# Kernel optimization log

Measured on AMD Instinct MI355X. Metric: run time of the kernel, lower is better.

## Reference

```python
import jax, jax.numpy as jnp
import numpy as np

DIM = 1024
HEADS = 16
DHEAD = 64
MAXLEN = 512
B = 8
N = 256   # sequence (x) length
M = 256   # memory (h) length; M + N <= MAXLEN
INNER = HEADS * DHEAD


def setup_inputs() -> dict:
    key = jax.random.key(0)
    ks = jax.random.split(key, 8)
    w = lambda k, shape: jax.random.normal(k, shape, jnp.float32) * 0.02
    return {
        "x": jax.random.normal(ks[0], (B, N, DIM), jnp.float32),
        "h": jax.random.normal(ks[1], (B, M, DIM), jnp.float32),
        "Wqkv": w(ks[2], (DIM, 3 * INNER)),
        "Wkr": w(ks[3], (DIM, INNER)),
        "R": jax.random.normal(ks[4], (2 * MAXLEN, DIM), jnp.float32),
        "u": jax.random.normal(ks[5], (DHEAD,), jnp.float32),
        "v": jax.random.normal(ks[6], (DHEAD,), jnp.float32),
        "Wout": w(ks[7], (INNER, DIM)),
        "max_len": MAXLEN,
    }


def reference(x, h, Wqkv, Wkr, R, u, v, Wout, max_len):
    b, n, dim = x.shape
    m = h.shape[1]
    t = m + n
    scale = DHEAD ** -0.5

    cat = jnp.concatenate([h, x], axis=1)                     # [b, t, dim]
    qkv = cat @ Wqkv                                          # [b, t, 3*inner]
    q, k, val = [s.reshape(b, t, HEADS, DHEAD).transpose(0, 2, 1, 3)
                 for s in jnp.split(qkv, 3, axis=-1)]          # [b, h, t, d]

    # shifts[i, j] = (j - i) mod 2L, sliced as in the torch buffer
    ar = jnp.arange(2 * max_len)
    shifts_full = (ar[None, :] - ar[:, None]) % (2 * max_len)
    shifts = shifts_full[:max_len, :max_len][m:m + n, :t]      # [n, t]

    kr = (R @ Wkr)[shifts]                                    # gather: [n, t, inner]
    kr = kr.reshape(n, t, HEADS, DHEAD).transpose(2, 0, 1, 3)  # [h, n, t, d]

    q = q[:, :, m:]                                           # [b, h, n, d]

    term_a = jnp.einsum('bhnd,bhmd->bhnm', q, k)
    term_b = jnp.einsum('bhnd,hnmd->bhnm', q, kr)
    term_c = jnp.einsum('d,bhmd->bhm', u, k)[:, :, None, :]    # broadcast over n
    term_d = jnp.einsum('d,hnmd->hnm', v, kr)[None]            # broadcast over b
    dots = (term_a + term_b + term_c + term_d) * scale         # [b, h, n, t]

    qi = jnp.arange(n)[:, None]
    jm = jnp.arange(m)[None, :]
    js = jnp.arange(n)[None, :]
    mem_mask = jnp.where(qi > jm, -jnp.inf, 0.0)               # [n, m]
    ar_mask = jnp.where(js > qi, -jnp.inf, 0.0)                # [n, n]
    bias = jnp.concatenate([mem_mask, ar_mask], axis=1)[None, None]  # [1,1,n,t]

    attn = jax.nn.softmax(dots + bias, axis=-1)
    out = jnp.einsum('bhnm,bhmd->bhnd', attn, val)             # [b, h, n, d]
    out = out.transpose(0, 2, 1, 3).reshape(b, n, INNER)
    return out @ Wout
```

## Files before the change

kernel.cpp:

```cpp
#include <hip/hip_runtime.h>
#include <hip/hip_bf16.h>
#include <math.h>

typedef unsigned short u16;
typedef short bf16x8 __attribute__((ext_vector_type(8)));
typedef float f32x4 __attribute__((ext_vector_type(4)));

__device__ __forceinline__ u16 f2b(float f) {
    __hip_bfloat16 h = __float2bfloat16(f);
    return *reinterpret_cast<u16*>(&h);
}
__device__ __forceinline__ float b2f(u16 v) {
    __hip_bfloat16 h;
    *reinterpret_cast<u16*>(&h) = v;
    return __bfloat162float(h);
}

__device__ __forceinline__ void gload_lds16(const void* g, void* l) {
    __builtin_amdgcn_global_load_lds(
        (const __attribute__((address_space(1))) void*)g,
        (__attribute__((address_space(3))) void*)l, 16, 0, 0);
}


struct EpiQKV4 {
    u16 *Q, *Kt, *Vt;
    __device__ void operator()(int rowp, int colp, f32x4 vals) const {
        int b = colp >> 9, pos = colp & 511;
        int sec = rowp >> 10, cc = rowp & 1023;
        int head = cc >> 6, d0 = cc & 63;
        ushort4 o;
        if (sec == 0) {
            if (pos < 256) return;
            o.x = f2b(vals[0] * 0.125f); o.y = f2b(vals[1] * 0.125f);
            o.z = f2b(vals[2] * 0.125f); o.w = f2b(vals[3] * 0.125f);
            *(ushort4*)(Q + (long)((head * 8 + b) * 256 + (pos - 256)) * 64 + d0) = o;
        } else {
            u16* dst = (sec == 1) ? Kt : Vt;
            o.x = f2b(vals[0]); o.y = f2b(vals[1]);
            o.z = f2b(vals[2]); o.w = f2b(vals[3]);
            *(ushort4*)(dst + (long)((b * 16 + head) * 512 + pos) * 64 + d0) = o;
        }
    }
};

struct EpiStoreBf {
    u16* C; long ldc; long strideZ;
    __device__ void operator()(int z, int row, int col, float val) const {
        C[(long)z * strideZ + (long)row * ldc + col] = f2b(val);
    }
};

struct EpiStoreF32 {
    float* C; long ldc;
    __device__ void operator()(int z, int row, int col, float val) const {
        C[(long)row * ldc + col] = val;
    }
};


template <typename Epi, bool AF32, bool ADDA, bool ROWMAP>
__device__ __forceinline__ void gemm_bt_body(char* smem, int bx, int by, int bz,
                                             const void* __restrict__ Av, int lda, long strideAz,
                                             const u16* __restrict__ B, int ldb, long strideBz,
                                             int K, Epi epi, const float* __restrict__ av) {
    constexpr int LDT = 56;
    u16* As = (u16*)smem;
    u16* Bs = As + 64 * LDT;
    int n0 = bx * 64, m0 = by * 64, z = bz;
    const u16* Bb = B + (long)z * strideBz + (long)n0 * ldb;
    int tid = threadIdx.x;
    int wave = tid >> 6, lane = tid & 63;
    int wm = wave >> 1, wn = wave & 1;
    int lrow = lane & 15, lquad = lane >> 4;
    int srow = tid >> 2, scol = (tid & 3) * 8;
    f32x4 acc[2][2] = {};
    for (int k0 = 0; k0 < K; k0 += 32) {
        if constexpr (AF32) {
            long arow = m0 + srow;
            if constexpr (ROWMAP) arow = (arow < 256) ? 768 + arow : 0;
            const float* src = (const float*)Av + (long)z * strideAz + arow * lda + k0 + scol;
            float4 f0 = *(const float4*)src;
            float4 f1 = *(const float4*)(src + 4);
            bf16x8 vv;
            vv[0] = (short)f2b(f0.x); vv[1] = (short)f2b(f0.y);
            vv[2] = (short)f2b(f0.z); vv[3] = (short)f2b(f0.w);
            vv[4] = (short)f2b(f1.x); vv[5] = (short)f2b(f1.y);
            vv[6] = (short)f2b(f1.z); vv[7] = (short)f2b(f1.w);
            *(bf16x8*)(As + srow * LDT + scol) = vv;
        } else {
            const u16* Ab = (const u16*)Av + (long)z * strideAz + (long)m0 * lda;
            *(bf16x8*)(As + srow * LDT + scol) = *(const bf16x8*)(Ab + (long)srow * lda + k0 + scol);
        }
        *(bf16x8*)(Bs + srow * LDT + scol) = *(const bf16x8*)(Bb + (long)srow * ldb + k0 + scol);
        __syncthreads();
        bf16x8 af[2], bfr[2];
        #pragma unroll
        for (int mt = 0; mt < 2; ++mt) {
            af[mt] = *(const bf16x8*)(As + (wm * 32 + mt * 16 + lrow) * LDT + lquad * 8);
            if constexpr (ADDA) {
                #pragma unroll
                for (int j = 0; j < 8; ++j)
                    af[mt][j] = (short)f2b(b2f((u16)af[mt][j]) + 0.125f * av[k0 + lquad * 8 + j]);
            }
        }
        #pragma unroll
        for (int nt = 0; nt < 2; ++nt)
            bfr[nt] = *(const bf16x8*)(Bs + (wn * 32 + nt * 16 + lrow) * LDT + lquad * 8);
        #pragma unroll
        for (int mt = 0; mt < 2; ++mt)
            #pragma unroll
            for (int nt = 0; nt < 2; ++nt)
                acc[mt][nt] = __builtin_amdgcn_mfma_f32_16x16x32_bf16(af[mt], bfr[nt], acc[mt][nt], 0, 0, 0);
        __syncthreads();
    }
    #pragma unroll
    for (int mt = 0; mt < 2; ++mt)
        #pragma unroll
        for (int nt = 0; nt < 2; ++nt)
            #pragma unroll
            for (int r = 0; r < 4; ++r) {
                int row = m0 + wm * 32 + mt * 16 + lquad * 4 + r;
                int col = n0 + wn * 32 + nt * 16 + lrow;
                epi(z, row, col, acc[mt][nt][r]);
            }
}

__global__ __launch_bounds__(256) void prep_kernel(const float* __restrict__ x,
                                                   const float* __restrict__ h,
                                                   u16* __restrict__ catBF,
                                                   const float* __restrict__ Wqkv, u16* __restrict__ WqkvT,
                                                   const float* __restrict__ Wkr,  u16* __restrict__ WkrT,
                                                   const float* __restrict__ Wout, u16* __restrict__ WoutT) {
    __shared__ float tile[32][33];
    int bid = blockIdx.x, tid = threadIdx.x;
    if (bid < 2048) {
        int idx = (bid * 256 + tid) * 8;
        int c = idx & 1023, r = idx >> 10;
        int b = r >> 9, pos = r & 511;
        const float* src = (pos < 256) ? h + ((long)(b * 256 + pos) * 1024 + c)
                                       : x + ((long)(b * 256 + pos - 256) * 1024 + c);
        float4 f0 = *(const float4*)src;
        float4 f1 = *(const float4*)(src + 4);
        bf16x8 vv;
        vv[0] = (short)f2b(f0.x); vv[1] = (short)f2b(f0.y);
        vv[2] = (short)f2b(f0.z); vv[3] = (short)f2b(f0.w);
        vv[4] = (short)f2b(f1.x); vv[5] = (short)f2b(f1.y);
        vv[6] = (short)f2b(f1.z); vv[7] = (short)f2b(f1.w);
        *(bf16x8*)(catBF + idx) = vv;
        return;
    }
    const float* W; u16* WT; int nb, kb;
    if (bid < 5120) {
        int w = bid - 2048;
        W = Wqkv; WT = WqkvT;
        nb = (w % 96) * 32; kb = (w / 96) * 32;
        int tx = tid & 31, ty = tid >> 5;
        #pragma unroll
        for (int i = 0; i < 32; i += 8)
            tile[ty + i][tx] = W[(long)(kb + ty + i) * 3072 + nb + tx];
    } else {
        int w = bid - 5120;
        if (w < 1024) { W = Wkr; WT = WkrT; }
        else          { W = Wout; WT = WoutT; w -= 1024; }
        nb = (w & 31) * 32; kb = (w >> 5) * 32;
        int tx = tid & 31, ty = tid >> 5;
        #pragma unroll
        for (int i = 0; i < 32; i += 8)
            tile[ty + i][tx] = W[(long)(kb + ty + i) * 1024 + nb + tx];
    }
    __syncthreads();
    int row = tid >> 3;
    int c4 = (tid & 7) * 4;
    ushort4 o;
    o.x = f2b(tile[c4 + 0][row]);
    o.y = f2b(tile[c4 + 1][row]);
    o.z = f2b(tile[c4 + 2][row]);
    o.w = f2b(tile[c4 + 3][row]);
    *(ushort4*)(WT + (long)(nb + row) * 1024 + kb + c4) = o;
}

__global__ __launch_bounds__(256) void qkv_rwg_kernel(const u16* __restrict__ A, const u16* __restrict__ B,
                                                      EpiQKV4 eq,
                                                      const float* __restrict__ R, const u16* __restrict__ WkrT,
                                                      u16* __restrict__ RWg) {
    __shared__ alignas(16) char smem[32768];
    int bid = blockIdx.x;
    if (bid >= 768) {
        int bid2 = bid - 768;
        gemm_bt_body<EpiStoreBf, true, false, true>(smem, bid2 & 15, bid2 >> 4, 0,
            (const void*)R, 1024, 0L, WkrT, 1024, 0L, 1024, EpiStoreBf{RWg, 1024, 0}, nullptr);
        return;
    }
    int n0 = (bid & 31) * 128, m0 = (bid >> 5) * 128;
    u16* As = (u16*)smem;
    u16* Bs = As + 8192;
    int tid = threadIdx.x, wave = tid >> 6, lane = tid & 63;
    int wm = wave >> 1, wn = wave & 1;
    int lrow = lane & 15, lquad = lane >> 4;
    const u16* Ab = A + (long)m0 * 1024;
    const u16* Bb = B + (long)n0 * 1024;
    f32x4 acc[4][4] = {};
    for (int k0 = 0; k0 < 1024; k0 += 64) {
        #pragma unroll
        for (int i = 0; i < 4; ++i) {
            int rowb = (i & 1) * 64 + (tid >> 2);
            int col = k0 + (i >> 1) * 32 + (tid & 3) * 8;
            gload_lds16(Ab + (long)rowb * 1024 + col, As + i * 2048 + tid * 8);
            gload_lds16(Bb + (long)rowb * 1024 + col, Bs + i * 2048 + tid * 8);
        }
        __syncthreads();
        #pragma unroll
        for (int ks = 0; ks < 2; ++ks) {
            bf16x8 af[4], bfr[4];
            #pragma unroll
            for (int mt = 0; mt < 4; ++mt)
                af[mt] = *(const bf16x8*)(As + ks * 4096 + (wm * 64 + mt * 16 + lrow) * 32 + lquad * 8);
            #pragma unroll
            for (int nt = 0; nt < 4; ++nt)
                bfr[nt] = *(const bf16x8*)(Bs + ks * 4096 + (wn * 64 + nt * 16 + lrow) * 32 + lquad * 8);
            #pragma unroll
            for (int mt = 0; mt < 4; ++mt)
                #pragma unroll
                for (int nt = 0; nt < 4; ++nt)
                    acc[mt][nt] = __builtin_amdgcn_mfma_f32_16x16x32_bf16(af[mt], bfr[nt], acc[mt][nt], 0, 0, 0);
        }
        __syncthreads();
    }
    #pragma unroll
    for (int mt = 0; mt < 4; ++mt)
        #pragma unroll
        for (int nt = 0; nt < 4; ++nt) {
            int rowp = m0 + wm * 64 + mt * 16 + lquad * 4;
            int colp = n0 + wn * 64 + nt * 16 + lrow;
            eq(rowp, colp, acc[mt][nt]);
        }
}

__global__ __launch_bounds__(256) void vtrans_qr_kernel(const u16* __restrict__ Vtmp, u16* __restrict__ VT,
                                                        const u16* __restrict__ Q, const u16* __restrict__ RWg,
                                                        u16* __restrict__ QR, const float* __restrict__ v) {
    __shared__ alignas(16) char smem[14336];
    int bid = blockIdx.x, tid = threadIdx.x;
    if (bid < 4096) {
        u16 (*tile)[34] = (u16(*)[34])smem;
        int t0 = (bid & 15) * 32, d0 = ((bid >> 4) & 1) * 32, bh = bid >> 5;
        int tx = tid & 31, ty = tid >> 5;
        const u16* src = Vtmp + (long)bh * 512 * 64;
        #pragma unroll
        for (int i = 0; i < 32; i += 8)
            tile[ty + i][tx] = src[(long)(t0 + ty + i) * 64 + d0 + tx];
        __syncthreads();
        u16* dst = VT + (long)bh * 64 * 512;
        #pragma unroll
        for (int i = 0; i < 32; i += 8)
            dst[(long)(d0 + ty + i) * 512 + t0 + tx] = tile[tx][ty + i];
        return;
    }
    int bid2 = bid - 4096;
    int bx = bid2 % 5;
    int rest = bid2 / 5;
    int by = rest & 31, bz = rest >> 5;
    gemm_bt_body<EpiStoreBf, false, true, false>(smem, bx, by, bz,
        (const void*)Q, 64, 2048L * 64, RWg, 1024, 64L, 64,
        EpiStoreBf{QR, 320, 2048L * 320}, v);
}

__global__ __launch_bounds__(256) void outproj_kernel(const u16* __restrict__ A,
                                                      const u16* __restrict__ B,
                                                      float* __restrict__ out) {
    __shared__ alignas(16) char smem[14336];
    gemm_bt_body<EpiStoreF32, false, false, false>(smem, blockIdx.x, blockIdx.y, 0,
        (const void*)A, 1024, 0L, B, 1024, 0L, 1024, EpiStoreF32{out, 1024}, nullptr);
}

__global__ __launch_bounds__(256, 4) void attn_kernel(const u16* __restrict__ Qs,
                                                      const u16* __restrict__ Kt,
                                                      const u16* __restrict__ VT,
                                                      const u16* __restrict__ QR,
                                                      const float* __restrict__ uvec,
                                                      u16* __restrict__ attnOut) {
    constexpr int LDSW = 328;
    __shared__ alignas(16) u16 SQ[32 * LDSW];
    __shared__ float red[2][4][32];
    int id = blockIdx.x;
    int bh = id & 127, it = id >> 7;
    int b = bh >> 4, h = bh & 15;
    int i0 = it * 32;
    int w0 = i0;
    int tid = threadIdx.x, wave = tid >> 6, lane = tid & 63;
    int lrow = lane & 15, lquad = lane >> 4;

    const u16* qrg = QR + ((long)h * 2048 + b * 256 + i0) * 320;
    #pragma unroll
    for (int kk = 0; kk < 5; ++kk) {
        int idx = tid + kk * 256;
        int row = idx / 40, c = idx - row * 40;
        *(bf16x8*)(SQ + row * LDSW + c * 8) = *(const bf16x8*)(qrg + row * 320 + c * 8);
    }

    bf16x8 aq[2][2];
    #pragma unroll
    for (int iu = 0; iu < 2; ++iu) {
        const u16* qbase = Qs + (long)((h * 8 + b) * 256 + i0 + iu * 16 + lrow) * 64;
        aq[iu][0] = *(const bf16x8*)(qbase + lquad * 8);
        aq[iu][1] = *(const bf16x8*)(qbase + 32 + lquad * 8);
        #pragma unroll
        for (int j = 0; j < 8; ++j) {
            aq[iu][0][j] = (short)f2b(b2f((u16)aq[iu][0][j]) + 0.125f * uvec[lquad * 8 + j]);
            aq[iu][1][j] = (short)f2b(b2f((u16)aq[iu][1][j]) + 0.125f * uvec[32 + lquad * 8 + j]);
        }
    }

    const u16* kbase = Kt + ((long)bh * 512 + w0 + wave * 80) * 64;
    bf16x8 bk0[5], bk1[5];
    #pragma unroll
    for (int t = 0; t < 5; ++t) {
        const u16* kp = kbase + (long)(t * 16 + lrow) * 64;
        bk0[t] = *(const bf16x8*)(kp + lquad * 8);
        bk1[t] = *(const bf16x8*)(kp + 32 + lquad * 8);
    }
    f32x4 acc[2][5];
    #pragma unroll
    for (int t = 0; t < 5; ++t)
        #pragma unroll
        for (int iu = 0; iu < 2; ++iu) {
            f32x4 a = {0.f, 0.f, 0.f, 0.f};
            a = __builtin_amdgcn_mfma_f32_16x16x32_bf16(aq[iu][0], bk0[t], a, 0, 0, 0);
            a = __builtin_amdgcn_mfma_f32_16x16x32_bf16(aq[iu][1], bk1[t], a, 0, 0, 0);
            acc[iu][t] = a;
        }
    __syncthreads();

    float m4[2][4];
    #pragma unroll
    for (int iu = 0; iu < 2; ++iu)
        #pragma unroll
        for (int r = 0; r < 4; ++r) m4[iu][r] = -1e30f;
    #pragma unroll
    for (int t = 0; t < 5; ++t) {
        int lj = wave * 80 + t * 16 + lrow;
        #pragma unroll
        for (int iu = 0; iu < 2; ++iu)
            #pragma unroll
            for (int r = 0; r < 4; ++r) {
                int rloc = iu * 16 + lquad * 4 + r;
                int d = lj - rloc;
                int dc = d < 0 ? 0 : (d > 256 ? 256 : d);
                bool ok = (unsigned)d <= 256u;
                float val = ok ? acc[iu][t][r] + b2f(SQ[rloc * LDSW + dc]) : -1e30f;
                acc[iu][t][r] = val;
                m4[iu][r] = fmaxf(m4[iu][r], val);
            }
    }
    #pragma unroll
    for (int iu = 0; iu < 2; ++iu)
        #pragma unroll
        for (int r = 0; r < 4; ++r) {
            #pragma unroll
            for (int off = 1; off < 16; off <<= 1)
                m4[iu][r] = fmaxf(m4[iu][r], __shfl_xor(m4[iu][r], off));
            if (lrow == 0) red[0][wave][iu * 16 + lquad * 4 + r] = m4[iu][r];
        }
    __syncthreads();

    float gmax[2][4];
    #pragma unroll
    for (int iu = 0; iu < 2; ++iu)
        #pragma unroll
        for (int r = 0; r < 4; ++r) {
            int row = iu * 16 + lquad * 4 + r;
            gmax[iu][r] = fmaxf(fmaxf(red[0][0][row], red[0][1][row]),
                                fmaxf(red[0][2][row], red[0][3][row]));
        }

    float s4[2][4] = {};
    #pragma unroll
    for (int t = 0; t < 5; ++t) {
        int lj = wave * 80 + t * 16 + lrow;
        #pragma unroll
        for (int iu = 0; iu < 2; ++iu)
            #pragma unroll
            for (int r = 0; r < 4; ++r) {
                float p = __expf(acc[iu][t][r] - gmax[iu][r]);
                s4[iu][r] += p;
                SQ[(iu * 16 + lquad * 4 + r) * LDSW + lj] = f2b(p);
            }
    }
    #pragma unroll
    for (int iu = 0; iu < 2; ++iu)
        #pragma unroll
        for (int r = 0; r < 4; ++r) {
            #pragma unroll
            for (int off = 1; off < 16; off <<= 1)
                s4[iu][r] += __shfl_xor(s4[iu][r], off);
            if (lrow == 0) red[1][wave][iu * 16 + lquad * 4 + r] = s4[iu][r];
        }
    __syncthreads();

    const u16* vbase = VT + ((long)bh * 64 + wave * 16 + lrow) * 512 + w0;
    f32x4 oacc[2] = {};
    bf16x8 vp[10];
    #pragma unroll
    for (int t = 0; t < 10; ++t)
        vp[t] = *(const bf16x8*)(vbase + t * 32 + lquad * 8);
    #pragma unroll
    for (int t = 0; t < 10; ++t)
        #pragma unroll
        for (int iu = 0; iu < 2; ++iu) {
            bf16x8 ap = *(const bf16x8*)(SQ + (iu * 16 + lrow) * LDSW + t * 32 + lquad * 8);
            oacc[iu] = __builtin_amdgcn_mfma_f32_16x16x32_bf16(ap, vp[t], oacc[iu], 0, 0, 0);
        }
    #pragma unroll
    for (int iu = 0; iu < 2; ++iu)
        #pragma unroll
        for (int r = 0; r < 4; ++r) {
            int row = iu * 16 + lquad * 4 + r;
            float inv = 1.0f / (red[1][0][row] + red[1][1][row] + red[1][2][row] + red[1][3][row]);
            attnOut[(long)(b * 256 + i0 + row) * 1024 + h * 64 + wave * 16 + lrow] = f2b(oacc[iu][r] * inv);
        }
}


extern "C" void kernel_launch(void* const* d_in, const int* in_sizes, int n_in,
                              void* d_out, int out_size, void* d_ws, size_t ws_size,
                              hipStream_t stream) {
    (void)in_sizes; (void)n_in; (void)out_size; (void)ws_size;
    const float* x    = (const float*)d_in[0];
    const float* h    = (const float*)d_in[1];
    const float* Wqkv = (const float*)d_in[2];
    const float* Wkr  = (const float*)d_in[3];
    const float* R    = (const float*)d_in[4];
    const float* u    = (const float*)d_in[5];
    const float* v    = (const float*)d_in[6];
    const float* Wout = (const float*)d_in[7];
    float* out = (float*)d_out;

    char* ws = (char*)d_ws;
    size_t off = 0;
    auto alloc = [&](size_t bytes) -> void* {
        void* p = ws + off;
        off = (off + bytes + 255) & ~(size_t)255;
        return p;
    };
    u16* catBF  = (u16*)alloc(4096L * 1024 * 2);
    u16* WqkvT  = (u16*)alloc(3072L * 1024 * 2);
    u16* WkrT   = (u16*)alloc(1024L * 1024 * 2);
    u16* WoutT  = (u16*)alloc(1024L * 1024 * 2);
    u16* RWg    = (u16*)alloc(320L * 1024 * 2);
    u16* Q      = (u16*)alloc(16L * 8 * 256 * 64 * 2);
    u16* Kt     = (u16*)alloc(8L * 16 * 512 * 64 * 2);
    u16* Vtmp   = (u16*)alloc(8L * 16 * 512 * 64 * 2);
    u16* VT     = (u16*)alloc(8L * 16 * 64 * 512 * 2);
    u16* QR     = (u16*)alloc(16L * 2048 * 320 * 2);
    u16* attnO  = (u16*)alloc(2048L * 1024 * 2);

    prep_kernel<<<7168, 256, 0, stream>>>(x, h, catBF, Wqkv, WqkvT, Wkr, WkrT, Wout, WoutT);
    qkv_rwg_kernel<<<848, 256, 0, stream>>>(WqkvT, catBF, EpiQKV4{Q, Kt, Vtmp}, R, WkrT, RWg);
    vtrans_qr_kernel<<<6656, 256, 0, stream>>>(Vtmp, VT, Q, RWg, QR, v);
    attn_kernel<<<1024, 256, 0, stream>>>(Q, Kt, VT, QR, u, attnO);
    outproj_kernel<<<dim3(16, 32), 256, 0, stream>>>(attnO, WoutT, out);
}
```

Baseline: 194.3 us.

## Skip unused memory-token Q tiles, double-buffer QKV GEMM, swizzle blocks

The QKV GEMM now computes the Q projection only for the sequence tokens, since Q for the memory tokens is never used. K and V are still computed for all tokens, which cuts the grid from 768 to 640 GEMM tiles. The k-loop is double-buffered in LDS with explicit vmcnt waits and barriers, so loads for the next tile overlap MFMA compute. Block indices are remapped so blocks spread across XCDs. The LDS use doubles to 64KB, which may lower occupancy.

New measurement: 185.6 us. -4.5%, faster.

```diff
diff --git a/kernel.cpp b/kernel.cpp
--- a/kernel.cpp
+++ b/kernel.cpp
@@ -184,49 +184,82 @@
                                                       EpiQKV4 eq,
                                                       const float* __restrict__ R, const u16* __restrict__ WkrT,
                                                       u16* __restrict__ RWg) {
-    __shared__ alignas(16) char smem[32768];
-    int bid = blockIdx.x;
-    if (bid >= 768) {
-        int bid2 = bid - 768;
+    __shared__ alignas(16) char smem[65536];
+    int bid0 = blockIdx.x;
+    if (bid0 >= 640) {
+        int bid2 = bid0 - 640;
         gemm_bt_body<EpiStoreBf, true, false, true>(smem, bid2 & 15, bid2 >> 4, 0,
             (const void*)R, 1024, 0L, WkrT, 1024, 0L, 1024, EpiStoreBf{RWg, 1024, 0}, nullptr);
         return;
     }
-    int n0 = (bid & 31) * 128, m0 = (bid >> 5) * 128;
-    u16* As = (u16*)smem;
-    u16* Bs = As + 8192;
+    int bid = (bid0 & 7) * 80 + (bid0 >> 3);
+    int m0, n0;
+    if (bid < 512) {
+        m0 = 1024 + (bid >> 5) * 128;
+        n0 = (bid & 31) * 128;
+    } else {
+        int q = bid - 512;
+        m0 = (q >> 4) * 128;
+        int c = q & 15;
+        n0 = (c >> 1) * 512 + 256 + (c & 1) * 128;
+    }
     int tid = threadIdx.x, wave = tid >> 6, lane = tid & 63;
     int wm = wave >> 1, wn = wave & 1;
     int lrow = lane & 15, lquad = lane >> 4;
     const u16* Ab = A + (long)m0 * 1024;
     const u16* Bb = B + (long)n0 * 1024;
     f32x4 acc[4][4] = {};
-    for (int k0 = 0; k0 < 1024; k0 += 64) {
+
+    auto stage = [&](int buf, int k0) {
+        u16* Asb = (u16*)smem + buf * 16384;
+        u16* Bsb = Asb + 8192;
         #pragma unroll
         for (int i = 0; i < 4; ++i) {
             int rowb = (i & 1) * 64 + (tid >> 2);
             int col = k0 + (i >> 1) * 32 + (tid & 3) * 8;
-            gload_lds16(Ab + (long)rowb * 1024 + col, As + i * 2048 + tid * 8);
-            gload_lds16(Bb + (long)rowb * 1024 + col, Bs + i * 2048 + tid * 8);
-        }
-        __syncthreads();
+            gload_lds16(Ab + (long)rowb * 1024 + col, Asb + i * 2048 + tid * 8);
+            gload_lds16(Bb + (long)rowb * 1024 + col, Bsb + i * 2048 + tid * 8);
+        }
+    };
+    auto compute = [&](int buf) {
+        u16* Asb = (u16*)smem + buf * 16384;
+        u16* Bsb = Asb + 8192;
         #pragma unroll
         for (int ks = 0; ks < 2; ++ks) {
             bf16x8 af[4], bfr[4];
             #pragma unroll
             for (int mt = 0; mt < 4; ++mt)
-                af[mt] = *(const bf16x8*)(As + ks * 4096 + (wm * 64 + mt * 16 + lrow) * 32 + lquad * 8);
+                af[mt] = *(const bf16x8*)(Asb + ks * 4096 + (wm * 64 + mt * 16 + lrow) * 32 + lquad * 8);
             #pragma unroll
             for (int nt = 0; nt < 4; ++nt)
-                bfr[nt] = *(const bf16x8*)(Bs + ks * 4096 + (wn * 64 + nt * 16 + lrow) * 32 + lquad * 8);
+                bfr[nt] = *(const bf16x8*)(Bsb + ks * 4096 + (wn * 64 + nt * 16 + lrow) * 32 + lquad * 8);
             #pragma unroll
             for (int mt = 0; mt < 4; ++mt)
                 #pragma unroll
                 for (int nt = 0; nt < 4; ++nt)
                     acc[mt][nt] = __builtin_amdgcn_mfma_f32_16x16x32_bf16(af[mt], bfr[nt], acc[mt][nt], 0, 0, 0);
         }
-        __syncthreads();
-    }
+    };
+
+    stage(0, 0);
+    stage(1, 64);
+    for (int t = 0; t < 15; ++t) {
+        asm volatile("s_waitcnt vmcnt(8)" ::: "memory");
+        __builtin_amdgcn_sched_barrier(0);
+        __builtin_amdgcn_s_barrier();
+        __builtin_amdgcn_sched_barrier(0);
+        compute(t & 1);
+        __builtin_amdgcn_sched_barrier(0);
+        __builtin_amdgcn_s_barrier();
+        __builtin_amdgcn_sched_barrier(0);
+        if (t < 14) stage(t & 1, (t + 2) * 64);
+    }
+    asm volatile("s_waitcnt vmcnt(0)" ::: "memory");
+    __builtin_amdgcn_sched_barrier(0);
+    __builtin_amdgcn_s_barrier();
+    __builtin_amdgcn_sched_barrier(0);
+    compute(1);
+
     #pragma unroll
     for (int mt = 0; mt < 4; ++mt)
         #pragma unroll
@@ -456,7 +489,7 @@
     u16* attnO  = (u16*)alloc(2048L * 1024 * 2);
 
     prep_kernel<<<7168, 256, 0, stream>>>(x, h, catBF, Wqkv, WqkvT, Wkr, WkrT, Wout, WoutT);
-    qkv_rwg_kernel<<<848, 256, 0, stream>>>(WqkvT, catBF, EpiQKV4{Q, Kt, Vtmp}, R, WkrT, RWg);
+    qkv_rwg_kernel<<<720, 256, 0, stream>>>(WqkvT, catBF, EpiQKV4{Q, Kt, Vtmp}, R, WkrT, RWg);
     vtrans_qr_kernel<<<6656, 256, 0, stream>>>(Vtmp, VT, Q, RWg, QR, v);
     attn_kernel<<<1024, 256, 0, stream>>>(Q, Kt, VT, QR, u, attnO);
     outproj_kernel<<<dim3(16, 32), 256, 0, stream>>>(attnO, WoutT, out);
```
